# Optimization experiments

Hardware: AMD Instinct MI355X
Metric: run time of the kernel (lower is better)

## Reference

```python
import jax, jax.numpy as jnp
import numpy as np

G = 16       # groups
GRID = 25    # hardcoded self.grid
EPS = 1e-5   # BatchNorm eps


def _gconv(x, w, pad):
    # x: (B, Cin, H, W), w: (Cout, Cin//G, kh, kw); grouped conv, stride 1
    return jax.lax.conv_general_dilated(
        x, w, window_strides=(1, 1), padding=[(pad, pad), (pad, pad)],
        feature_group_count=G)


def _bn_relu(h, g, b, m, v):
    # h: (G, B, C, H, W); per-group-instance BN params: (G, C). Inference BN.
    scale = (g / jnp.sqrt(v + EPS))[:, None, :, None, None]
    return jax.nn.relu((h - m[:, None, :, None, None]) * scale + b[:, None, :, None, None])


def setup_inputs() -> dict:
    key = jax.random.key(0)
    ks = jax.random.split(key, 11)
    B, C, H, W = 2, 256, 24, 24
    AC = GRID * C  # 6400 affinity channels
    return {
        "x":  jax.random.normal(ks[0], (B, C, H, W), jnp.float32),
        "W1": jax.random.normal(ks[1], (G, C, C // G, 3, 3), jnp.float32) * 0.05,
        "g1": jax.random.uniform(ks[2], (G, C), jnp.float32, 0.5, 1.5),
        "b1": jax.random.normal(ks[3], (G, C), jnp.float32) * 0.1,
        "m1": jax.random.normal(ks[4], (G, C), jnp.float32) * 0.1,
        "v1": jax.random.uniform(ks[5], (G, C), jnp.float32, 0.5, 1.5),
        "W2": jax.random.normal(ks[6], (G, AC, C // G, 1, 1), jnp.float32) * 0.05,
        "g2": jax.random.uniform(ks[7], (G, AC), jnp.float32, 0.5, 1.5),
        "b2": jax.random.normal(ks[8], (G, AC), jnp.float32) * 0.1,
        "m2": jax.random.normal(ks[9], (G, AC), jnp.float32) * 0.1,
        "v2": jax.random.uniform(ks[10], (G, AC), jnp.float32, 0.5, 1.5),
    }


def reference(x, W1, g1, b1, m1, v1, W2, g2, b2, m2, v2):
    B, C, H, W = x.shape
    Cg = C // G
    # 16 independent grouped 3x3 convs over the same input, batched via vmap
    h1 = jax.vmap(lambda w: _gconv(x, w, 1))(W1)          # (G, B, C, H, W)
    h1 = _bn_relu(h1, g1, b1, m1, v1)
    # grouped 1x1 conv with padding=1 (faithful to source -> spatial grows to H+2, W+2)
    a = jax.vmap(lambda h, w: _gconv(h, w, 1))(h1, W2)    # (G, B, 25C, H+2, W+2)
    a = _bn_relu(a, g2, b2, m2, v2)
    pooled = a.mean(axis=(-2, -1))                        # adaptive avg pool -> (G, B, 25C)
    xv = pooled.reshape(G, B, G, GRID * Cg)               # (G, B, G, 25*Cg)
    aff = jnp.einsum('ibkm,iblm->ibkl', xv, xv)           # (G, B, G, G) = theta @ phi
    idx = jnp.arange(G)
    aff_i = aff[idx, :, idx, :] / G                       # aff[:, i], /N  -> (G, B, G)
    ex = h1.reshape(G, B, G, Cg * H * W)
    # torch.matmul((B,G), (B,G,M)) broadcasts 2-D lhs -> (B, B, M); kept faithfully
    z = jnp.einsum('ipk,iqkm->ipqm', aff_i, ex)           # (G, B, B, Cg*H*W)
    z = z.reshape(G, B, B, Cg, H, W).transpose(1, 0, 2, 3, 4, 5)
    return z.reshape(B, G * B * Cg, H, W)                 # (B, B*C, H, W)
```

## Files before the change

kernel.cpp:

```cpp
#include <hip/hip_runtime.h>
#include <hip/hip_bf16.h>


typedef __attribute__((ext_vector_type(8))) short short8;
typedef __attribute__((ext_vector_type(4))) float f32x4;

static __device__ __forceinline__ short f2bf(float x) {
    unsigned u = __float_as_uint(x);
    unsigned r = (u + 0x7fffu + ((u >> 16) & 1u)) >> 16;
    return (short)r;
}

#define WA_OFF  33696
#define WLB_OFF 23040
#define B2_OFF  35840
#define PS_OFF  37440
#define ZP_OFF  43840
#define SMEM_BYTES 43856

__global__ __launch_bounds__(256) void k12_fused(
    const float* __restrict__ xin,
    const float* __restrict__ W1,
    const float* __restrict__ g1, const float* __restrict__ b1,
    const float* __restrict__ m1, const float* __restrict__ v1,
    const float* __restrict__ W2,
    const float* __restrict__ g2, const float* __restrict__ b2,
    const float* __restrict__ m2, const float* __restrict__ v2,
    float* __restrict__ h1f,
    float* __restrict__ pooled)
{
    __shared__ __align__(16) char smem[SMEM_BYTES];
    short* xs    = (short*)smem;
    short* wAp   = (short*)(smem + WA_OFF);
    short* hsb   = (short*)smem;
    short* wlb   = (short*)(smem + WLB_OFF);
    float* bias2 = (float*)(smem + B2_OFF);
    float* psum  = (float*)(smem + PS_OFF);
    __shared__ float scale1[16], bias1[16];

    int bid  = blockIdx.x;
    int hsel = bid & 1;
    int core = bid >> 1;
    int i = core >> 5, b = (core >> 4) & 1, g = core & 15;
    int t = threadIdx.x;

    int* xz = (int*)xs;
    for (int idx = t; idx < 27*26*12; idx += 256) xz[idx] = 0;
    if (t < 4) ((int*)(smem + ZP_OFF))[t] = 0;
    if (t < 16) {
        int c = i*256 + g*16 + t;
        float sc = g1[c] * rsqrtf(v1[c] + 1e-5f);
        scale1[t] = sc;
        bias1[t]  = b1[c] - m1[c] * sc;
    }
    __syncthreads();

    const float* xb = &xin[(b*256 + g*16)*576];
    for (int idx = t; idx < 9216; idx += 256) {
        int ci = idx / 576; int s = idx - ci*576;
        int y = s / 24; int x = s - y*24;
        xs[((y+1)*26 + (x+1))*24 + ci] = f2bf(xb[idx]);
    }
    const float* wb = &W1[(i*256 + g*16)*144];
    for (int idx = t; idx < 2560; idx += 256) {
        int kk = idx >> 9, rem = idx & 511, co = rem >> 5, k = rem & 31;
        int tap = 2*kk + (k >> 4), ci = k & 15;
        float val = (tap < 9) ? wb[co*144 + ci*9 + tap] * scale1[co] : 0.f;
        wAp[(kk*16 + co)*40 + k] = f2bf(val);
    }
    __syncthreads();

    int l = t & 63, w = t >> 6;
    int quad = l >> 4, rc = l & 15;

    f32x4 dreg[9];
    {
        int ci0 = (quad & 1) * 8;
        short8 afr[5];
#pragma unroll
        for (int kk = 0; kk < 5; kk++)
            afr[kk] = *(const short8*)&wAp[(kk*16 + rc)*40 + quad*8];
        f32x4 cb1 = *(const f32x4*)&bias1[quad*4];

        const int offE[5] = {0, 48, 648, 1248, 1296};
        const int offO[5] = {24, 624, 672, 1272, 1872};
        int off[5];
#pragma unroll
        for (int kk = 0; kk < 5; kk++) off[kk] = (quad >= 2) ? offO[kk] : offE[kk];

#pragma unroll
        for (int tt = 0; tt < 9; tt++) {
            int s = (w*9 + tt)*16 + rc;
            int y = s / 24; int x = s - y*24;
            int base = (y*26 + x)*24 + ci0;
            f32x4 acc = cb1;
#pragma unroll
            for (int kk = 0; kk < 5; kk++) {
                short8 bf = *(const short8*)&xs[base + off[kk]];
                acc = __builtin_amdgcn_mfma_f32_16x16x32_bf16(afr[kk], bf, acc, 0, 0, 0);
            }
#pragma unroll
            for (int r = 0; r < 4; r++) acc[r] = fmaxf(acc[r], 0.f);
            dreg[tt] = acc;
        }
    }
    __syncthreads();

    {
        float* hout = &h1f[((i*2 + b)*256 + g*16)*576];
#pragma unroll
        for (int tt = 0; tt < 9; tt++) {
            int s = (w*9 + tt)*16 + rc;
            f32x4 acc = dreg[tt];
            unsigned p0 = (unsigned)(unsigned short)f2bf(acc[0]) |
                          ((unsigned)(unsigned short)f2bf(acc[1]) << 16);
            unsigned p1 = (unsigned)(unsigned short)f2bf(acc[2]) |
                          ((unsigned)(unsigned short)f2bf(acc[3]) << 16);
            uint2 pk = {p0, p1};
            *(uint2*)&hsb[s*20 + quad*4] = pk;
            if (hsel == 0) {
#pragma unroll
                for (int r = 0; r < 4; r++)
                    hout[(quad*4 + r)*576 + s] = acc[r];
            }
        }
    }

    int m_lo = hsel ? 208 : 0;
    int m_hi = hsel ? 400 : 208;
    for (int m = m_lo + t; m < m_hi; m += 256) {
        int o = i*6400 + g*400 + m;
        float s2 = g2[o] * rsqrtf(v2[o] + 1e-5f);
        bias2[m] = b2[o] - m2[o] * s2;
        const float4* wr = (const float4*)&W2[o*16];
#pragma unroll
        for (int q = 0; q < 4; q++) {
            float4 wv = wr[q];
            wlb[m*16 + q*4 + 0] = f2bf(wv.x * s2);
            wlb[m*16 + q*4 + 1] = f2bf(wv.y * s2);
            wlb[m*16 + q*4 + 2] = f2bf(wv.z * s2);
            wlb[m*16 + q*4 + 3] = f2bf(wv.w * s2);
        }
    }
    __syncthreads();

    {
        int q8 = (quad & 1) * 8;
        short8 af2[9];
#pragma unroll
        for (int u = 0; u < 9; u++) {
            int boff = (l < 32) ? ((((w*9 + u)*16 + rc)*20 + q8)*2) : ZP_OFF;
            af2[u] = *(const short8*)(smem + boff);
        }
        int mt_lo = hsel ? 13 : 0;
        int mt_hi = hsel ? 25 : 13;
        for (int mt = mt_lo; mt < mt_hi; mt++) {
            int m0 = mt*16;
            int woff = (l < 32) ? (WLB_OFF + ((m0 + rc)*16 + q8)*2) : ZP_OFF;
            short8 wf = *(const short8*)(smem + woff);
            float be = bias2[m0 + rc];
            f32x4 cb = {be, be, be, be};

            f32x4 accv = {0.f, 0.f, 0.f, 0.f};
#pragma unroll
            for (int u = 0; u < 9; u++) {
                f32x4 d = __builtin_amdgcn_mfma_f32_16x16x32_bf16(af2[u], wf, cb, 0, 0, 0);
#pragma unroll
                for (int r = 0; r < 4; r++)
                    accv[r] += fmaxf(d[r], 0.f);
            }
            float a = (accv[0] + accv[1]) + (accv[2] + accv[3]);
            a += __shfl_xor(a, 16);
            a += __shfl_xor(a, 32);
            if (l < 16)
                psum[w*400 + m0 + l] = a;
        }
    }
    __syncthreads();

    const float inv = 1.f / 676.f;
    for (int m = m_lo + t; m < m_hi; m += 256) {
        float s = psum[0*400+m] + psum[1*400+m] + psum[2*400+m] + psum[3*400+m];
        float be = bias2[m];
        pooled[(i*2+b)*6400 + g*400 + m] = (s + 100.f * fmaxf(be, 0.f)) * inv;
    }
}

__global__ __launch_bounds__(256) void k34_out(const float* __restrict__ pooled,
                                               const float* __restrict__ h1f,
                                               float* __restrict__ out)
{
    __shared__ float parts[256];
    __shared__ float av[2][16];
    int bid = blockIdx.x;
    int i = bid >> 5, q = (bid >> 4) & 1, cg = bid & 15;
    int t = threadIdx.x;

    {
        int pl = t >> 3;
        int u  = t & 7;
        int p = pl >> 4, lidx = pl & 15;
        const float* pb = &pooled[(i*2 + p)*6400];
        const float* pt = &pb[i*400];
        const float* pl2 = &pb[lidx*400];
        float s = 0.f;
        for (int m = u*50; m < u*50 + 50; m++) s = fmaf(pt[m], pl2[m], s);
        parts[t] = s;
    }
    __syncthreads();
    if (t < 32) {
        float s = 0.f;
#pragma unroll
        for (int u = 0; u < 8; u++) s += parts[t*8 + u];
        av[t >> 4][t & 15] = s * (1.f/16.f);
    }
    __syncthreads();

    const float* hb = &h1f[((i*2 + q)*256 + cg)*576];
    int ch = i*32 + q*16 + cg;
    for (int s = t; s < 576; s += 256) {
        float acc0 = 0.f, acc1 = 0.f;
#pragma unroll
        for (int k = 0; k < 16; k++) {
            float v = hb[k*9216 + s];
            acc0 = fmaf(av[0][k], v, acc0);
            acc1 = fmaf(av[1][k], v, acc1);
        }
        out[ch*576 + s]         = acc0;
        out[(512 + ch)*576 + s] = acc1;
    }
}

extern "C" void kernel_launch(void* const* d_in, const int* in_sizes, int n_in,
                              void* d_out, int out_size, void* d_ws, size_t ws_size,
                              hipStream_t stream)
{
    const float* x  = (const float*)d_in[0];
    const float* W1 = (const float*)d_in[1];
    const float* g1 = (const float*)d_in[2];
    const float* b1 = (const float*)d_in[3];
    const float* m1 = (const float*)d_in[4];
    const float* v1 = (const float*)d_in[5];
    const float* W2 = (const float*)d_in[6];
    const float* g2 = (const float*)d_in[7];
    const float* b2 = (const float*)d_in[8];
    const float* m2 = (const float*)d_in[9];
    const float* v2 = (const float*)d_in[10];

    float* h1f    = (float*)d_ws;
    float* pooled = h1f + 16*2*256*576;

    float* out = (float*)d_out;

    hipLaunchKernelGGL(k12_fused, dim3(1024), dim3(256), 0, stream,
                       x, W1, g1, b1, m1, v1, W2, g2, b2, m2, v2, h1f, pooled);
    hipLaunchKernelGGL(k34_out,   dim3(512),  dim3(256), 0, stream,
                       pooled, h1f, out);
}
```

Baseline: 125.8 us.

## Split fused conv kernel by spatial row bands and reduce pooled sums atomically

Each (i,b,g) work item is now split into three blocks that each cover 8 output rows, where before two blocks split the 1x1-conv channel range and each redundantly computed the full 3x3 conv. Each block loads only its input row band plus halo, computes its share of h1, and does all 400 affinity channels over its spatial slice. Partial pooled sums go straight to global memory with atomicAdd into a buffer that is zeroed by a memset, which replaces the shared psum buffer and the final reduction pass. This cuts redundant conv work and shared memory use so more blocks fit per CU. It costs an extra memset launch, atomic traffic, repeated W2 staging in every block, and a float summation order that is no longer fixed.

```diff
diff --git a/kernel.cpp b/kernel.cpp
--- a/kernel.cpp
+++ b/kernel.cpp
@@ -11,12 +11,11 @@
     return (short)r;
 }
 
-#define WA_OFF  33696
-#define WLB_OFF 23040
-#define B2_OFF  35840
-#define PS_OFF  37440
-#define ZP_OFF  43840
-#define SMEM_BYTES 43856
+#define WA_OFF  12480
+#define WLB_OFF 7680
+#define B2_OFF  23680
+#define ZP_OFF  25280
+#define SMEM_BYTES 25296
 
 __global__ __launch_bounds__(256) void k12_fused(
     const float* __restrict__ xin,
@@ -35,17 +34,17 @@
     short* hsb   = (short*)smem;
     short* wlb   = (short*)(smem + WLB_OFF);
     float* bias2 = (float*)(smem + B2_OFF);
-    float* psum  = (float*)(smem + PS_OFF);
     __shared__ float scale1[16], bias1[16];
 
     int bid  = blockIdx.x;
-    int hsel = bid & 1;
-    int core = bid >> 1;
+    int hsel = bid >> 9;
+    int core = bid & 511;
     int i = core >> 5, b = (core >> 4) & 1, g = core & 15;
     int t = threadIdx.x;
+    int r0 = hsel << 3;
 
     int* xz = (int*)xs;
-    for (int idx = t; idx < 27*26*12; idx += 256) xz[idx] = 0;
+    for (int idx = t; idx < 3120; idx += 256) xz[idx] = 0;
     if (t < 4) ((int*)(smem + ZP_OFF))[t] = 0;
     if (t < 16) {
         int c = i*256 + g*16 + t;
@@ -56,10 +55,12 @@
     __syncthreads();
 
     const float* xb = &xin[(b*256 + g*16)*576];
-    for (int idx = t; idx < 9216; idx += 256) {
-        int ci = idx / 576; int s = idx - ci*576;
-        int y = s / 24; int x = s - y*24;
-        xs[((y+1)*26 + (x+1))*24 + ci] = f2bf(xb[idx]);
+    for (int idx = t; idx < 3840; idx += 256) {
+        int ci = idx / 240; int rem = idx - ci*240;
+        int lr = rem / 24;  int x = rem - lr*24;
+        int r = r0 + lr - 1;
+        if ((unsigned)r < 24u)
+            xs[(lr*26 + x + 1)*24 + ci] = f2bf(xb[ci*576 + r*24 + x]);
     }
     const float* wb = &W1[(i*256 + g*16)*144];
     for (int idx = t; idx < 2560; idx += 256) {
@@ -73,7 +74,7 @@
     int l = t & 63, w = t >> 6;
     int quad = l >> 4, rc = l & 15;
 
-    f32x4 dreg[9];
+    f32x4 dreg[3];
     {
         int ci0 = (quad & 1) * 8;
         short8 afr[5];
@@ -89,10 +90,10 @@
         for (int kk = 0; kk < 5; kk++) off[kk] = (quad >= 2) ? offO[kk] : offE[kk];
 
 #pragma unroll
-        for (int tt = 0; tt < 9; tt++) {
-            int s = (w*9 + tt)*16 + rc;
-            int y = s / 24; int x = s - y*24;
-            int base = (y*26 + x)*24 + ci0;
+        for (int tt = 0; tt < 3; tt++) {
+            int sl = (w*3 + tt)*16 + rc;
+            int ly = sl / 24; int x = sl - ly*24;
+            int base = (ly*26 + x)*24 + ci0;
             f32x4 acc = cb1;
 #pragma unroll
             for (int kk = 0; kk < 5; kk++) {
@@ -107,28 +108,24 @@
     __syncthreads();
 
     {
-        float* hout = &h1f[((i*2 + b)*256 + g*16)*576];
-#pragma unroll
-        for (int tt = 0; tt < 9; tt++) {
-            int s = (w*9 + tt)*16 + rc;
+        float* hout = &h1f[((i*2 + b)*256 + g*16)*576 + hsel*192];
+#pragma unroll
+        for (int tt = 0; tt < 3; tt++) {
+            int sl = (w*3 + tt)*16 + rc;
             f32x4 acc = dreg[tt];
             unsigned p0 = (unsigned)(unsigned short)f2bf(acc[0]) |
                           ((unsigned)(unsigned short)f2bf(acc[1]) << 16);
             unsigned p1 = (unsigned)(unsigned short)f2bf(acc[2]) |
                           ((unsigned)(unsigned short)f2bf(acc[3]) << 16);
             uint2 pk = {p0, p1};
-            *(uint2*)&hsb[s*20 + quad*4] = pk;
-            if (hsel == 0) {
-#pragma unroll
-                for (int r = 0; r < 4; r++)
-                    hout[(quad*4 + r)*576 + s] = acc[r];
-            }
-        }
-    }
-
-    int m_lo = hsel ? 208 : 0;
-    int m_hi = hsel ? 400 : 208;
-    for (int m = m_lo + t; m < m_hi; m += 256) {
+            *(uint2*)&hsb[sl*20 + quad*4] = pk;
+#pragma unroll
+            for (int r = 0; r < 4; r++)
+                hout[(quad*4 + r)*576 + sl] = acc[r];
+        }
+    }
+
+    for (int m = t; m < 400; m += 256) {
         int o = i*6400 + g*400 + m;
         float s2 = g2[o] * rsqrtf(v2[o] + 1e-5f);
         bias2[m] = b2[o] - m2[o] * s2;
@@ -136,34 +133,35 @@
 #pragma unroll
         for (int q = 0; q < 4; q++) {
             float4 wv = wr[q];
-            wlb[m*16 + q*4 + 0] = f2bf(wv.x * s2);
-            wlb[m*16 + q*4 + 1] = f2bf(wv.y * s2);
-            wlb[m*16 + q*4 + 2] = f2bf(wv.z * s2);
-            wlb[m*16 + q*4 + 3] = f2bf(wv.w * s2);
+            wlb[m*20 + q*4 + 0] = f2bf(wv.x * s2);
+            wlb[m*20 + q*4 + 1] = f2bf(wv.y * s2);
+            wlb[m*20 + q*4 + 2] = f2bf(wv.z * s2);
+            wlb[m*20 + q*4 + 3] = f2bf(wv.w * s2);
         }
     }
     __syncthreads();
 
     {
         int q8 = (quad & 1) * 8;
-        short8 af2[9];
-#pragma unroll
-        for (int u = 0; u < 9; u++) {
-            int boff = (l < 32) ? ((((w*9 + u)*16 + rc)*20 + q8)*2) : ZP_OFF;
+        short8 af2[3];
+#pragma unroll
+        for (int u = 0; u < 3; u++) {
+            int boff = (l < 32) ? ((((w*3 + u)*16 + rc)*20 + q8)*2) : ZP_OFF;
             af2[u] = *(const short8*)(smem + boff);
         }
-        int mt_lo = hsel ? 13 : 0;
-        int mt_hi = hsel ? 25 : 13;
-        for (int mt = mt_lo; mt < mt_hi; mt++) {
+        const float inv = 1.f / 676.f;
+        float* pout = &pooled[(i*2 + b)*6400 + g*400];
+        bool bmaster = (hsel == 0) && (w == 0);
+        for (int mt = 0; mt < 25; mt++) {
             int m0 = mt*16;
-            int woff = (l < 32) ? (WLB_OFF + ((m0 + rc)*16 + q8)*2) : ZP_OFF;
+            int woff = (l < 32) ? (WLB_OFF + ((m0 + rc)*20 + q8)*2) : ZP_OFF;
             short8 wf = *(const short8*)(smem + woff);
             float be = bias2[m0 + rc];
             f32x4 cb = {be, be, be, be};
 
             f32x4 accv = {0.f, 0.f, 0.f, 0.f};
 #pragma unroll
-            for (int u = 0; u < 9; u++) {
+            for (int u = 0; u < 3; u++) {
                 f32x4 d = __builtin_amdgcn_mfma_f32_16x16x32_bf16(af2[u], wf, cb, 0, 0, 0);
 #pragma unroll
                 for (int r = 0; r < 4; r++)
@@ -172,17 +170,10 @@
             float a = (accv[0] + accv[1]) + (accv[2] + accv[3]);
             a += __shfl_xor(a, 16);
             a += __shfl_xor(a, 32);
+            if (bmaster) a += 100.f * fmaxf(be, 0.f);
             if (l < 16)
-                psum[w*400 + m0 + l] = a;
-        }
-    }
-    __syncthreads();
-
-    const float inv = 1.f / 676.f;
-    for (int m = m_lo + t; m < m_hi; m += 256) {
-        float s = psum[0*400+m] + psum[1*400+m] + psum[2*400+m] + psum[3*400+m];
-        float be = bias2[m];
-        pooled[(i*2+b)*6400 + g*400 + m] = (s + 100.f * fmaxf(be, 0.f)) * inv;
+                atomicAdd(&pout[m0 + l], a * inv);
+        }
     }
 }
 
@@ -252,7 +243,9 @@
 
     float* out = (float*)d_out;
 
-    hipLaunchKernelGGL(k12_fused, dim3(1024), dim3(256), 0, stream,
+    hipMemsetAsync(pooled, 0, 16*2*6400*sizeof(float), stream);
+
+    hipLaunchKernelGGL(k12_fused, dim3(1536), dim3(256), 0, stream,
                        x, W1, g1, b1, m1, v1, W2, g2, b2, m2, v2, h1f, pooled);
     hipLaunchKernelGGL(k34_out,   dim3(512),  dim3(256), 0, stream,
                        pooled, h1f, out);
```

New measurement: 124.2 us. No clear change (-1.3%).

## Store h1 intermediate as bf16 and stop splitting conv work across block pairs

Applied to the files above, without the earlier changes.

The h1 intermediate is now written to the workspace as bf16 rather than fp32, and the output kernel widens it back to float on load, halving that intermediate's traffic. The fused conv kernel stops launching two blocks per (i,b,g) that each recompute the 3x3 conv and take half of the 1x1 channels; one block now handles all 400 channels. Per-wave partial pool sums are merged with shared-memory atomics instead of a 4-way psum array. This removes the duplicated conv and input staging but halves the block count and serialises more work per block, and it lowers h1 precision in the final product.

```diff
diff --git a/kernel.cpp b/kernel.cpp
--- a/kernel.cpp
+++ b/kernel.cpp
@@ -5,18 +5,20 @@
 typedef __attribute__((ext_vector_type(8))) short short8;
 typedef __attribute__((ext_vector_type(4))) float f32x4;
 
-static __device__ __forceinline__ short f2bf(float x) {
+static __device__ __forceinline__ unsigned short f2bf(float x) {
     unsigned u = __float_as_uint(x);
     unsigned r = (u + 0x7fffu + ((u >> 16) & 1u)) >> 16;
-    return (short)r;
-}
-
-#define WA_OFF  33696
-#define WLB_OFF 23040
-#define B2_OFF  35840
-#define PS_OFF  37440
-#define ZP_OFF  43840
-#define SMEM_BYTES 43856
+    return (unsigned short)r;
+}
+
+#define WA_OFF   33696
+#define WLB_OFF  23040
+#define B2_OFF   35840
+#define PACC_OFF 37440
+#define ZP_OFF   40096
+#define S1_OFF   40112
+#define BB1_OFF  40176
+#define SMEM_BYTES 40240
 
 __global__ __launch_bounds__(256) void k12_fused(
     const float* __restrict__ xin,
@@ -26,7 +28,7 @@
     const float* __restrict__ W2,
     const float* __restrict__ g2, const float* __restrict__ b2,
     const float* __restrict__ m2, const float* __restrict__ v2,
-    float* __restrict__ h1f,
+    unsigned short* __restrict__ h1b,
     float* __restrict__ pooled)
 {
     __shared__ __align__(16) char smem[SMEM_BYTES];
@@ -35,13 +37,12 @@
     short* hsb   = (short*)smem;
     short* wlb   = (short*)(smem + WLB_OFF);
     float* bias2 = (float*)(smem + B2_OFF);
-    float* psum  = (float*)(smem + PS_OFF);
-    __shared__ float scale1[16], bias1[16];
-
-    int bid  = blockIdx.x;
-    int hsel = bid & 1;
-    int core = bid >> 1;
-    int i = core >> 5, b = (core >> 4) & 1, g = core & 15;
+    float* pacc  = (float*)(smem + PACC_OFF);
+    float* scale1 = (float*)(smem + S1_OFF);
+    float* bias1  = (float*)(smem + BB1_OFF);
+
+    int bid = blockIdx.x;
+    int i = bid >> 5, b = (bid >> 4) & 1, g = bid & 15;
     int t = threadIdx.x;
 
     int* xz = (int*)xs;
@@ -59,14 +60,14 @@
     for (int idx = t; idx < 9216; idx += 256) {
         int ci = idx / 576; int s = idx - ci*576;
         int y = s / 24; int x = s - y*24;
-        xs[((y+1)*26 + (x+1))*24 + ci] = f2bf(xb[idx]);
+        xs[((y+1)*26 + (x+1))*24 + ci] = (short)f2bf(xb[idx]);
     }
     const float* wb = &W1[(i*256 + g*16)*144];
     for (int idx = t; idx < 2560; idx += 256) {
         int kk = idx >> 9, rem = idx & 511, co = rem >> 5, k = rem & 31;
         int tap = 2*kk + (k >> 4), ci = k & 15;
         float val = (tap < 9) ? wb[co*144 + ci*9 + tap] * scale1[co] : 0.f;
-        wAp[(kk*16 + co)*40 + k] = f2bf(val);
+        wAp[(kk*16 + co)*40 + k] = (short)f2bf(val);
     }
     __syncthreads();
 
@@ -107,28 +108,26 @@
     __syncthreads();
 
     {
-        float* hout = &h1f[((i*2 + b)*256 + g*16)*576];
+        unsigned short* hout = &h1b[((i*2 + b)*256 + g*16)*576];
 #pragma unroll
         for (int tt = 0; tt < 9; tt++) {
             int s = (w*9 + tt)*16 + rc;
             f32x4 acc = dreg[tt];
-            unsigned p0 = (unsigned)(unsigned short)f2bf(acc[0]) |
-                          ((unsigned)(unsigned short)f2bf(acc[1]) << 16);
-            unsigned p1 = (unsigned)(unsigned short)f2bf(acc[2]) |
-                          ((unsigned)(unsigned short)f2bf(acc[3]) << 16);
+            unsigned short e0 = f2bf(acc[0]), e1 = f2bf(acc[1]);
+            unsigned short e2 = f2bf(acc[2]), e3 = f2bf(acc[3]);
+            unsigned p0 = (unsigned)e0 | ((unsigned)e1 << 16);
+            unsigned p1 = (unsigned)e2 | ((unsigned)e3 << 16);
             uint2 pk = {p0, p1};
             *(uint2*)&hsb[s*20 + quad*4] = pk;
-            if (hsel == 0) {
-#pragma unroll
-                for (int r = 0; r < 4; r++)
-                    hout[(quad*4 + r)*576 + s] = acc[r];
-            }
-        }
-    }
-
-    int m_lo = hsel ? 208 : 0;
-    int m_hi = hsel ? 400 : 208;
-    for (int m = m_lo + t; m < m_hi; m += 256) {
+            hout[(quad*4 + 0)*576 + s] = e0;
+            hout[(quad*4 + 1)*576 + s] = e1;
+            hout[(quad*4 + 2)*576 + s] = e2;
+            hout[(quad*4 + 3)*576 + s] = e3;
+        }
+    }
+
+    for (int m = t; m < 400; m += 256) {
+        pacc[m] = 0.f;
         int o = i*6400 + g*400 + m;
         float s2 = g2[o] * rsqrtf(v2[o] + 1e-5f);
         bias2[m] = b2[o] - m2[o] * s2;
@@ -136,10 +135,10 @@
 #pragma unroll
         for (int q = 0; q < 4; q++) {
             float4 wv = wr[q];
-            wlb[m*16 + q*4 + 0] = f2bf(wv.x * s2);
-            wlb[m*16 + q*4 + 1] = f2bf(wv.y * s2);
-            wlb[m*16 + q*4 + 2] = f2bf(wv.z * s2);
-            wlb[m*16 + q*4 + 3] = f2bf(wv.w * s2);
+            wlb[m*16 + q*4 + 0] = (short)f2bf(wv.x * s2);
+            wlb[m*16 + q*4 + 1] = (short)f2bf(wv.y * s2);
+            wlb[m*16 + q*4 + 2] = (short)f2bf(wv.z * s2);
+            wlb[m*16 + q*4 + 3] = (short)f2bf(wv.w * s2);
         }
     }
     __syncthreads();
@@ -152,9 +151,7 @@
             int boff = (l < 32) ? ((((w*9 + u)*16 + rc)*20 + q8)*2) : ZP_OFF;
             af2[u] = *(const short8*)(smem + boff);
         }
-        int mt_lo = hsel ? 13 : 0;
-        int mt_hi = hsel ? 25 : 13;
-        for (int mt = mt_lo; mt < mt_hi; mt++) {
+        for (int mt = 0; mt < 25; mt++) {
             int m0 = mt*16;
             int woff = (l < 32) ? (WLB_OFF + ((m0 + rc)*16 + q8)*2) : ZP_OFF;
             short8 wf = *(const short8*)(smem + woff);
@@ -173,21 +170,21 @@
             a += __shfl_xor(a, 16);
             a += __shfl_xor(a, 32);
             if (l < 16)
-                psum[w*400 + m0 + l] = a;
+                atomicAdd(&pacc[m0 + l], a);
         }
     }
     __syncthreads();
 
     const float inv = 1.f / 676.f;
-    for (int m = m_lo + t; m < m_hi; m += 256) {
-        float s = psum[0*400+m] + psum[1*400+m] + psum[2*400+m] + psum[3*400+m];
+    for (int m = t; m < 400; m += 256) {
         float be = bias2[m];
-        pooled[(i*2+b)*6400 + g*400 + m] = (s + 100.f * fmaxf(be, 0.f)) * inv;
+        pooled[(i*2+b)*6400 + g*400 + m] =
+            (pacc[m] + 100.f * fmaxf(be, 0.f)) * inv;
     }
 }
 
 __global__ __launch_bounds__(256) void k34_out(const float* __restrict__ pooled,
-                                               const float* __restrict__ h1f,
+                                               const unsigned short* __restrict__ h1b,
                                                float* __restrict__ out)
 {
     __shared__ float parts[256];
@@ -216,13 +213,13 @@
     }
     __syncthreads();
 
-    const float* hb = &h1f[((i*2 + q)*256 + cg)*576];
+    const unsigned short* hb = &h1b[((i*2 + q)*256 + cg)*576];
     int ch = i*32 + q*16 + cg;
     for (int s = t; s < 576; s += 256) {
         float acc0 = 0.f, acc1 = 0.f;
 #pragma unroll
         for (int k = 0; k < 16; k++) {
-            float v = hb[k*9216 + s];
+            float v = __uint_as_float((unsigned)hb[k*9216 + s] << 16);
             acc0 = fmaf(av[0][k], v, acc0);
             acc1 = fmaf(av[1][k], v, acc1);
         }
@@ -247,13 +244,13 @@
     const float* m2 = (const float*)d_in[9];
     const float* v2 = (const float*)d_in[10];
 
-    float* h1f    = (float*)d_ws;
-    float* pooled = h1f + 16*2*256*576;
+    unsigned short* h1b = (unsigned short*)d_ws;
+    float* pooled = (float*)(h1b + 16*2*256*576);
 
     float* out = (float*)d_out;
 
-    hipLaunchKernelGGL(k12_fused, dim3(1024), dim3(256), 0, stream,
-                       x, W1, g1, b1, m1, v1, W2, g2, b2, m2, v2, h1f, pooled);
-    hipLaunchKernelGGL(k34_out,   dim3(512),  dim3(256), 0, stream,
-                       pooled, h1f, out);
-}
+    hipLaunchKernelGGL(k12_fused, dim3(512), dim3(256), 0, stream,
+                       x, W1, g1, b1, m1, v1, W2, g2, b2, m2, v2, h1b, pooled);
+    hipLaunchKernelGGL(k34_out,   dim3(512), dim3(256), 0, stream,
+                       pooled, h1b, out);
+}
```

Measured after the change: 119.0 us. 1.06x faster.
